# Optimization experiments

Hardware: AMD Instinct MI355X
Metric: run time of the kernel (lower is better)

Reference implementation:

```python
import jax, jax.numpy as jnp
import numpy as np

B, L, C = 4, 16384, 512   # batch, tokens (128x128 grid), dim
NH, WS = 8, 8             # num_heads, window grid (ws)
HD = C // NH              # head_dim = 64


def setup_inputs() -> dict:
    key = jax.random.key(0)
    k1, k2, k3, k4, k5 = jax.random.split(key, 5)
    return {
        "q":   jax.random.normal(k1, (B, L, C), dtype=jnp.float32),
        "kv":  jax.random.normal(k2, (B, L, C), dtype=jnp.float32),
        "Wq":  jax.random.normal(k3, (C, C), dtype=jnp.float32) * 0.02,
        "Wkv": jax.random.normal(k4, (C, 2 * C), dtype=jnp.float32) * 0.02,
        "Wfc": jax.random.normal(k5, (C, C), dtype=jnp.float32) * 0.02,
    }


def reference(q, kv, Wq, Wkv, Wfc):
    Bq, Lq, Cd = q.shape
    Lkv = kv.shape[1]
    nh, hd, ws = NH, Cd // NH, WS
    scale = hd ** (-0.5)
    hw_q = int(round(Lq ** 0.5))   # 128
    hw_k = int(round(Lkv ** 0.5))
    sq, sk = hw_q // ws, hw_k // ws  # window side lengths (16)

    qp = q @ Wq                                   # [B, Lq, C]
    kvp = (kv @ Wkv).reshape(Bq, Lkv, 2, Cd)
    k, v = kvp[:, :, 0], kvp[:, :, 1]             # [B, Lkv, C]

    def window(x, s):
        # [B, hw, hw, C] -> [B, ws*ws windows, heads, s*s tokens, hd]
        x = x.reshape(Bq, ws, s, ws, s, Cd).transpose(0, 1, 3, 2, 4, 5)
        x = x.reshape(Bq, ws * ws, s * s, nh, hd)
        return x.transpose(0, 1, 3, 2, 4)

    qw = window(qp, sq)   # [B, W, H, sq*sq, hd]
    kw = window(k, sk)    # [B, W, H, sk*sk, hd]
    vw = window(v, sk)

    attn = jnp.einsum('bwhqd,bwhkd->bwhqk', qw, kw) * scale
    attn = jax.nn.softmax(attn, axis=-1)
    o = jnp.einsum('bwhqk,bwhkd->bwhqd', attn, vw)  # [B, W, H, sq*sq, hd]

    # inverse window partition
    o = o.transpose(0, 1, 3, 2, 4).reshape(Bq, ws, ws, sq, sq, Cd)
    o = o.transpose(0, 1, 3, 2, 4, 5).reshape(Bq, Lq, Cd)
    return o @ Wfc
```

## Files before the change

kernel.cpp:

```cpp
#include <hip/hip_runtime.h>
#include <stdint.h>

#define BB 4
#define LL 16384
#define CC 512
#define MM (BB * LL)

typedef unsigned short u16;
typedef __bf16 bf16x8 __attribute__((ext_vector_type(8)));
typedef float f32x4 __attribute__((ext_vector_type(4)));
typedef u16 u16x8 __attribute__((ext_vector_type(8)));
typedef u16 u16x4 __attribute__((ext_vector_type(4)));

__device__ __forceinline__ u16 f2bf(float f) {
  return __builtin_bit_cast(u16, (__bf16)f);
}

__device__ __forceinline__ void gl_lds16(const void* g, void* l) {
  __builtin_amdgcn_global_load_lds((const __attribute__((address_space(1))) void*)g,
                                   (__attribute__((address_space(3))) void*)l,
                                   16, 0, 0);
}

__global__ __launch_bounds__(256) void prep_kernel(
    const float* __restrict__ q, const float* __restrict__ kv,
    const float* __restrict__ Wq, const float* __restrict__ Wkv,
    const float* __restrict__ Wfc, u16* __restrict__ qo, u16* __restrict__ kvo,
    u16* __restrict__ Wq_t, u16* __restrict__ Wkv_t, u16* __restrict__ Wfc_t) {
  __shared__ float tile[64][65];
  const int bid = blockIdx.x, tid = threadIdx.x;

  if (bid < 4096) {
    const int half = bid >> 11;
    const float* src = half ? kv : q;
    u16* dst = half ? kvo : qo;
    const int n16 = MM * CC / 16;
    const int stride = 2048 * 256;
    for (int i = (bid & 2047) * 256 + tid; i < n16; i += stride) {
      f32x4 a0 = reinterpret_cast<const f32x4*>(src)[4 * i + 0];
      f32x4 a1 = reinterpret_cast<const f32x4*>(src)[4 * i + 1];
      f32x4 a2 = reinterpret_cast<const f32x4*>(src)[4 * i + 2];
      f32x4 a3 = reinterpret_cast<const f32x4*>(src)[4 * i + 3];
      u16x8 o0, o1;
      o0[0] = f2bf(a0[0]); o0[1] = f2bf(a0[1]); o0[2] = f2bf(a0[2]); o0[3] = f2bf(a0[3]);
      o0[4] = f2bf(a1[0]); o0[5] = f2bf(a1[1]); o0[6] = f2bf(a1[2]); o0[7] = f2bf(a1[3]);
      o1[0] = f2bf(a2[0]); o1[1] = f2bf(a2[1]); o1[2] = f2bf(a2[2]); o1[3] = f2bf(a2[3]);
      o1[4] = f2bf(a3[0]); o1[5] = f2bf(a3[1]); o1[6] = f2bf(a3[2]); o1[7] = f2bf(a3[3]);
      reinterpret_cast<u16x8*>(dst)[2 * i + 0] = o0;
      reinterpret_cast<u16x8*>(dst)[2 * i + 1] = o1;
    }
    return;
  }

  const int wb = bid - 4096;
  const float* W; u16* Wt; int N, ti;
  if (wb < 64)       { W = Wq;  Wt = Wq_t;  N = 512;  ti = wb; }
  else if (wb < 192) { W = Wkv; Wt = Wkv_t; N = 1024; ti = wb - 64; }
  else               { W = Wfc; Wt = Wfc_t; N = 512;  ti = wb - 192; }
  const int ntn = N >> 6;
  const int kt = ti / ntn, nt = ti % ntn;
  const int k0 = kt << 6, n0 = nt << 6;
  {
    const int r = tid >> 4, c4 = tid & 15;
#pragma unroll
    for (int e = 0; e < 4; ++e) {
      int row = r + e * 16;
      f32x4 v = *reinterpret_cast<const f32x4*>(&W[(size_t)(k0 + row) * N + n0 + c4 * 4]);
      tile[row][c4 * 4 + 0] = v[0]; tile[row][c4 * 4 + 1] = v[1];
      tile[row][c4 * 4 + 2] = v[2]; tile[row][c4 * 4 + 3] = v[3];
    }
  }
  __syncthreads();
  {
    const int n = tid >> 2, qd = tid & 3;
#pragma unroll
    for (int e = 0; e < 2; ++e) {
      int c = qd * 2 + e;
      u16x8 o;
#pragma unroll
      for (int j = 0; j < 8; ++j) o[j] = f2bf(tile[c * 8 + j][n]);
      *reinterpret_cast<u16x8*>(&Wt[(size_t)(n0 + n) * 512 + k0 + c * 8]) = o;
    }
  }
}

template <bool OUT_F32>
__global__ __launch_bounds__(512, 2) void gemm256(const u16* __restrict__ A,
                                                  const u16* __restrict__ Bt,
                                                  void* __restrict__ Cp,
                                                  int M, int N, int K) {
  __shared__ __align__(16) u16 Al[3][16384];
  __shared__ __align__(16) u16 Bl[2][16384];
  const int nbn = N >> 8;
  const int nwg = gridDim.x;
  const int bid0 = blockIdx.x;
  const int cpx = nwg >> 3;
  const int bid = (bid0 & 7) * cpx + (bid0 >> 3);
  const int bm = bid / nbn, bn = bid % nbn;
  const size_t row0 = (size_t)bm << 8, col0 = (size_t)bn << 8;
  const int tid = threadIdx.x, lane = tid & 63;
  const int wv = tid >> 6, wm = wv >> 2, wn = wv & 3;
  const int ro = lane & 15, g4 = lane >> 4;
  const int NT = K >> 6;

  const int ci0 = tid, ci1 = tid + 512;
  const int r0 = ci0 >> 3, g0 = (ci0 & 7) ^ (r0 & 7);
  const int r1 = ci1 >> 3, g1 = (ci1 & 7) ^ (r1 & 7);

  auto stageA = [&](int half, int kt, u16* L) {
    gl_lds16(A + (row0 + half * 128 + r0) * (size_t)K + kt * 64 + g0 * 8, L + half * 8192 + ci0 * 8);
    gl_lds16(A + (row0 + half * 128 + r1) * (size_t)K + kt * 64 + g1 * 8, L + half * 8192 + ci1 * 8);
  };
  auto stageB = [&](int half, int kt, u16* L) {
    gl_lds16(Bt + (col0 + half * 128 + r0) * (size_t)K + kt * 64 + g0 * 8, L + half * 8192 + ci0 * 8);
    gl_lds16(Bt + (col0 + half * 128 + r1) * (size_t)K + kt * 64 + g1 * 8, L + half * 8192 + ci1 * 8);
  };

  const int aB = (wm * 128 + ro) * 64;
  const int bB = (wn * 64 + ro) * 64;
  const int sw0 = (g4 ^ (ro & 7)) * 8;
  const int sw1 = ((g4 + 4) ^ (ro & 7)) * 8;

  auto ldf = [&](const u16* p) { return *reinterpret_cast<const bf16x8*>(p); };

  f32x4 acc[8][4] = {};

  stageA(0, 0, Al[0]); stageA(1, 0, Al[0]);
  stageB(0, 0, Bl[0]); stageB(1, 0, Bl[0]);
  stageA(0, 1, Al[1]); stageA(1, 1, Al[1]);
  stageB(0, 1, Bl[1]); stageB(1, 1, Bl[1]);
  asm volatile("s_waitcnt vmcnt(8)" ::: "memory");
  __builtin_amdgcn_s_barrier();

  u16* Acur = Al[0]; u16* Anxt = Al[1]; u16* Asta = Al[2];
  u16* Bcur = Bl[0]; u16* Bnxt = Bl[1];

  for (int u = 0; u < NT; ++u) {
    const bool st = (u + 2) < NT;
    bf16x8 bfr[4][2], af[2][2];

#pragma unroll
    for (int n = 0; n < 4; ++n) {
      bfr[n][0] = ldf(Bcur + bB + n * 1024 + sw0);
      bfr[n][1] = ldf(Bcur + bB + n * 1024 + sw1);
    }
    af[0][0] = ldf(Acur + aB + sw0);        af[0][1] = ldf(Acur + aB + sw1);
    af[1][0] = ldf(Acur + aB + 1024 + sw0); af[1][1] = ldf(Acur + aB + 1024 + sw1);
    if (st) stageA(0, u + 2, Asta);
    __builtin_amdgcn_s_barrier();
    asm volatile("s_waitcnt lgkmcnt(0)" ::: "memory");
    __builtin_amdgcn_sched_barrier(0);
    __builtin_amdgcn_s_setprio(1);
#pragma unroll
    for (int m = 0; m < 2; ++m)
#pragma unroll
      for (int n = 0; n < 4; ++n) {
        acc[m][n] = __builtin_amdgcn_mfma_f32_16x16x32_bf16(af[m][0], bfr[n][0], acc[m][n], 0, 0, 0);
        acc[m][n] = __builtin_amdgcn_mfma_f32_16x16x32_bf16(af[m][1], bfr[n][1], acc[m][n], 0, 0, 0);
      }
    __builtin_amdgcn_s_setprio(0);
    __builtin_amdgcn_s_barrier();

#pragma unroll
    for (int ph = 1; ph < 4; ++ph) {
      af[0][0] = ldf(Acur + aB + (2 * ph) * 1024 + sw0);
      af[0][1] = ldf(Acur + aB + (2 * ph) * 1024 + sw1);
      af[1][0] = ldf(Acur + aB + (2 * ph + 1) * 1024 + sw0);
      af[1][1] = ldf(Acur + aB + (2 * ph + 1) * 1024 + sw1);
      if (ph == 1) { if (st) { stageA(1, u + 2, Asta); stageB(0, u + 2, Bcur); } }
      else if (ph == 2) { if (st) stageB(1, u + 2, Bcur); }
      __builtin_amdgcn_s_barrier();
      asm volatile("s_waitcnt lgkmcnt(0)" ::: "memory");
      __builtin_amdgcn_sched_barrier(0);
      __builtin_amdgcn_s_setprio(1);
#pragma unroll
      for (int m = 0; m < 2; ++m)
#pragma unroll
        for (int n = 0; n < 4; ++n) {
          acc[2 * ph + m][n] =
              __builtin_amdgcn_mfma_f32_16x16x32_bf16(af[m][0], bfr[n][0], acc[2 * ph + m][n], 0, 0, 0);
          acc[2 * ph + m][n] =
              __builtin_amdgcn_mfma_f32_16x16x32_bf16(af[m][1], bfr[n][1], acc[2 * ph + m][n], 0, 0, 0);
        }
      __builtin_amdgcn_s_setprio(0);
      if (ph == 3) {
        if (st) asm volatile("s_waitcnt vmcnt(8)" ::: "memory");
        else    asm volatile("s_waitcnt vmcnt(0)" ::: "memory");
      }
      __builtin_amdgcn_s_barrier();
    }

    u16* ta = Acur; Acur = Anxt; Anxt = Asta; Asta = ta;
    u16* tb = Bcur; Bcur = Bnxt; Bnxt = tb;
  }

#pragma unroll
  for (int m = 0; m < 8; ++m)
#pragma unroll
    for (int n = 0; n < 4; ++n)
#pragma unroll
      for (int j = 0; j < 4; ++j) {
        size_t r = row0 + wm * 128 + m * 16 + g4 * 4 + j;
        size_t c = col0 + wn * 64 + n * 16 + ro;
        if (OUT_F32)
          reinterpret_cast<float*>(Cp)[r * N + c] = acc[m][n][j];
        else
          reinterpret_cast<u16*>(Cp)[r * N + c] = f2bf(acc[m][n][j]);
      }
}

__global__ __launch_bounds__(512, 4) void attn_kernel(const u16* __restrict__ qp,
                                                      const u16* __restrict__ kvp,
                                                      u16* __restrict__ o) {
  __shared__ __align__(16) u16 Kl[256 * 64];
  __shared__ __align__(16) u16 Vt[64 * 256];
  __shared__ __align__(16) u16 Pl[8 * 1024];
  const int bid = blockIdx.x;
  const int h = bid & 7, w = (bid >> 3) & 63, b = bid >> 9;
  const int w1 = w >> 3, w2 = w & 7;
  const int tid = threadIdx.x, lane = tid & 63, wv = tid >> 6;

  auto lrow = [&](int t) { return (w1 * 16 + (t >> 4)) * 128 + w2 * 16 + (t & 15); };

#pragma unroll
  for (int p = 0; p < 4; ++p) {
    int ci = tid + p * 512;
    int r = ci >> 3, g = (ci & 7) ^ (r & 7);
    gl_lds16(kvp + ((size_t)(b * LL + lrow(r))) * 1024 + h * 64 + g * 8, Kl + ci * 8);
  }
  {
    const int tk = tid >> 1, half = tid & 1;
    const size_t base = ((size_t)(b * LL + lrow(tk))) * 1024 + 512 + h * 64 + half * 32;
#pragma unroll
    for (int c = 0; c < 4; ++c) {
      u16x8 vx = *reinterpret_cast<const u16x8*>(kvp + base + c * 8);
#pragma unroll
      for (int e = 0; e < 8; ++e) {
        int d = half * 32 + c * 8 + e;
        Vt[d * 256 + (((tk >> 3) ^ (d & 7)) * 8) + (tk & 7)] = vx[e];
      }
    }
  }
  __syncthreads();

  const int ro = lane & 15;
  const int g4 = lane >> 4;
  const float scale = 0.125f;
  const int swA = (g4 ^ (ro & 7)) * 8;
  const int swB = ((g4 + 4) ^ (ro & 7)) * 8;
  u16* PW = Pl + wv * 1024;

  auto ldf = [&](const u16* p) { return *reinterpret_cast<const bf16x8*>(p); };

#pragma unroll
  for (int rt = 0; rt < 2; ++rt) {
    const int tq = 32 * wv + 16 * rt + ro;
    const size_t qbase = ((size_t)(b * LL + lrow(tq))) * 512 + h * 64 + g4 * 8;
    const bf16x8 qf0 = *reinterpret_cast<const bf16x8*>(qp + qbase);
    const bf16x8 qf1 = *reinterpret_cast<const bf16x8*>(qp + qbase + 32);

    f32x4 sa[16] = {};
    __builtin_amdgcn_s_setprio(1);
#pragma unroll
    for (int ct = 0; ct < 16; ++ct) {
      bf16x8 kf0 = ldf(Kl + (16 * ct + ro) * 64 + swA);
      bf16x8 kf1 = ldf(Kl + (16 * ct + ro) * 64 + swB);
      sa[ct] = __builtin_amdgcn_mfma_f32_16x16x32_bf16(qf0, kf0, sa[ct], 0, 0, 0);
      sa[ct] = __builtin_amdgcn_mfma_f32_16x16x32_bf16(qf1, kf1, sa[ct], 0, 0, 0);
    }
    __builtin_amdgcn_s_setprio(0);

#pragma unroll
    for (int j = 0; j < 4; ++j) {
      float m = -1e30f;
#pragma unroll
      for (int ct = 0; ct < 16; ++ct) m = fmaxf(m, sa[ct][j]);
      m = fmaxf(m, __shfl_xor(m, 1));
      m = fmaxf(m, __shfl_xor(m, 2));
      m = fmaxf(m, __shfl_xor(m, 4));
      m = fmaxf(m, __shfl_xor(m, 8));
      m *= scale;
      float s = 0.f;
#pragma unroll
      for (int ct = 0; ct < 16; ++ct) {
        float p = __expf(sa[ct][j] * scale - m);
        sa[ct][j] = p;
        s += p;
      }
      s += __shfl_xor(s, 1);
      s += __shfl_xor(s, 2);
      s += __shfl_xor(s, 4);
      s += __shfl_xor(s, 8);
      float inv = 1.f / s;
#pragma unroll
      for (int ct = 0; ct < 16; ++ct) sa[ct][j] *= inv;
    }

    f32x4 oacc[4] = {};
#pragma unroll
    for (int kh = 0; kh < 4; ++kh) {
#pragma unroll
      for (int c = 0; c < 4; ++c)
#pragma unroll
        for (int j = 0; j < 4; ++j) {
          int rq = g4 * 4 + j;
          PW[rq * 64 + (((2 * c + (ro >> 3)) ^ (rq & 7)) * 8) + (ro & 7)] =
              f2bf(sa[kh * 4 + c][j]);
        }
      __builtin_amdgcn_s_setprio(1);
#pragma unroll
      for (int ks = 0; ks < 2; ++ks) {
        bf16x8 pf = ldf(PW + ro * 64 + (((ks * 4 + g4) ^ (ro & 7)) * 8));
        const int kkg = kh * 2 + ks;
#pragma unroll
        for (int cd = 0; cd < 4; ++cd) {
          bf16x8 vf = ldf(Vt + (16 * cd + ro) * 256 + (((kkg * 4 + g4) ^ (ro & 7)) * 8));
          oacc[cd] = __builtin_amdgcn_mfma_f32_16x16x32_bf16(pf, vf, oacc[cd], 0, 0, 0);
        }
      }
      __builtin_amdgcn_s_setprio(0);
    }

#pragma unroll
    for (int cd = 0; cd < 4; ++cd)
#pragma unroll
      for (int j = 0; j < 4; ++j) {
        int t = 32 * wv + 16 * rt + g4 * 4 + j;
        int d = 16 * cd + ro;
        o[((size_t)(b * LL + lrow(t))) * 512 + h * 64 + d] = f2bf(oacc[cd][j]);
      }
  }
}

extern "C" void kernel_launch(void* const* d_in, const int* in_sizes, int n_in,
                              void* d_out, int out_size, void* d_ws, size_t ws_size,
                              hipStream_t stream) {
  const float* q = (const float*)d_in[0];
  const float* kv = (const float*)d_in[1];
  const float* Wq = (const float*)d_in[2];
  const float* Wkv = (const float*)d_in[3];
  const float* Wfc = (const float*)d_in[4];
  float* out = (float*)d_out;
  char* ws = (char*)d_ws;

  u16* q_bf  = (u16*)(ws + 0);
  u16* kv_bf = (u16*)(ws + 67108864);
  u16* qp    = (u16*)(ws + 134217728);
  u16* kvp   = (u16*)(ws + 201326592);
  u16* Wq_t  = (u16*)(ws + 335544320);
  u16* Wkv_t = (u16*)(ws + 336068608);
  u16* Wfc_t = (u16*)(ws + 337117184);
  u16* o_buf = q_bf;

  prep_kernel<<<4352, 256, 0, stream>>>(q, kv, Wq, Wkv, Wfc, q_bf, kv_bf, Wq_t, Wkv_t, Wfc_t);

  gemm256<false><<<(MM / 256) * (CC / 256), 512, 0, stream>>>(q_bf, Wq_t, qp, MM, CC, CC);
  gemm256<false><<<(MM / 256) * (2 * CC / 256), 512, 0, stream>>>(kv_bf, Wkv_t, kvp, MM, 2 * CC, CC);

  attn_kernel<<<BB * 64 * 8, 512, 0, stream>>>(qp, kvp, o_buf);

  gemm256<true><<<(MM / 256) * (CC / 256), 512, 0, stream>>>(o_buf, Wfc_t, out, MM, CC, CC);
}
```

Before: 356.3 us.

## Make GEMM persistent with cross-tile prefetch pipeline and nontemporal prep loads

The GEMM kernel becomes persistent: 256 workgroups each process several consecutive output tiles. The LDS prefetch pipeline now continues across tile boundaries, so loads for the next tile's first k-steps overlap the current tile's tail and epilogue. This removes per-tile launch and prologue/drain bubbles. It also hard-codes K=512, which limits generality. Separately, the fp32→bf16 conversion in the prep kernel uses nontemporal loads to avoid polluting the cache with streaming input.

```diff
diff --git a/kernel.cpp b/kernel.cpp
--- a/kernel.cpp
+++ b/kernel.cpp
@@ -37,10 +37,11 @@
     const int n16 = MM * CC / 16;
     const int stride = 2048 * 256;
     for (int i = (bid & 2047) * 256 + tid; i < n16; i += stride) {
-      f32x4 a0 = reinterpret_cast<const f32x4*>(src)[4 * i + 0];
-      f32x4 a1 = reinterpret_cast<const f32x4*>(src)[4 * i + 1];
-      f32x4 a2 = reinterpret_cast<const f32x4*>(src)[4 * i + 2];
-      f32x4 a3 = reinterpret_cast<const f32x4*>(src)[4 * i + 3];
+      const f32x4* sp = reinterpret_cast<const f32x4*>(src) + 4 * i;
+      f32x4 a0 = __builtin_nontemporal_load(sp + 0);
+      f32x4 a1 = __builtin_nontemporal_load(sp + 1);
+      f32x4 a2 = __builtin_nontemporal_load(sp + 2);
+      f32x4 a3 = __builtin_nontemporal_load(sp + 3);
       u16x8 o0, o1;
       o0[0] = f2bf(a0[0]); o0[1] = f2bf(a0[1]); o0[2] = f2bf(a0[2]); o0[3] = f2bf(a0[3]);
       o0[4] = f2bf(a1[0]); o0[5] = f2bf(a1[1]); o0[6] = f2bf(a1[2]); o0[7] = f2bf(a1[3]);
@@ -88,32 +89,30 @@
 __global__ __launch_bounds__(512, 2) void gemm256(const u16* __restrict__ A,
                                                   const u16* __restrict__ Bt,
                                                   void* __restrict__ Cp,
-                                                  int M, int N, int K) {
+                                                  int N, int TPB, int nbnl) {
+  constexpr int K = 512;
+  constexpr int NT = 8;
   __shared__ __align__(16) u16 Al[3][16384];
   __shared__ __align__(16) u16 Bl[2][16384];
-  const int nbn = N >> 8;
-  const int nwg = gridDim.x;
   const int bid0 = blockIdx.x;
-  const int cpx = nwg >> 3;
-  const int bid = (bid0 & 7) * cpx + (bid0 >> 3);
-  const int bm = bid / nbn, bn = bid % nbn;
-  const size_t row0 = (size_t)bm << 8, col0 = (size_t)bn << 8;
+  const int bid = (bid0 & 7) * 32 + (bid0 >> 3);
+  const int T0 = bid * TPB;
+  const int taumax = TPB * NT;
   const int tid = threadIdx.x, lane = tid & 63;
   const int wv = tid >> 6, wm = wv >> 2, wn = wv & 3;
   const int ro = lane & 15, g4 = lane >> 4;
-  const int NT = K >> 6;
 
   const int ci0 = tid, ci1 = tid + 512;
   const int r0 = ci0 >> 3, g0 = (ci0 & 7) ^ (r0 & 7);
   const int r1 = ci1 >> 3, g1 = (ci1 & 7) ^ (r1 & 7);
 
-  auto stageA = [&](int half, int kt, u16* L) {
-    gl_lds16(A + (row0 + half * 128 + r0) * (size_t)K + kt * 64 + g0 * 8, L + half * 8192 + ci0 * 8);
-    gl_lds16(A + (row0 + half * 128 + r1) * (size_t)K + kt * 64 + g1 * 8, L + half * 8192 + ci1 * 8);
+  auto stageA = [&](int half, size_t row0s, int us, u16* L) {
+    gl_lds16(A + (row0s + half * 128 + r0) * (size_t)K + us * 64 + g0 * 8, L + half * 8192 + ci0 * 8);
+    gl_lds16(A + (row0s + half * 128 + r1) * (size_t)K + us * 64 + g1 * 8, L + half * 8192 + ci1 * 8);
   };
-  auto stageB = [&](int half, int kt, u16* L) {
-    gl_lds16(Bt + (col0 + half * 128 + r0) * (size_t)K + kt * 64 + g0 * 8, L + half * 8192 + ci0 * 8);
-    gl_lds16(Bt + (col0 + half * 128 + r1) * (size_t)K + kt * 64 + g1 * 8, L + half * 8192 + ci1 * 8);
+  auto stageB = [&](int half, size_t col0s, int us, u16* L) {
+    gl_lds16(Bt + (col0s + half * 128 + r0) * (size_t)K + us * 64 + g0 * 8, L + half * 8192 + ci0 * 8);
+    gl_lds16(Bt + (col0s + half * 128 + r1) * (size_t)K + us * 64 + g1 * 8, L + half * 8192 + ci1 * 8);
   };
 
   const int aB = (wm * 128 + ro) * 64;
@@ -122,53 +121,43 @@
   const int sw1 = ((g4 + 4) ^ (ro & 7)) * 8;
 
   auto ldf = [&](const u16* p) { return *reinterpret_cast<const bf16x8*>(p); };
+  auto trow = [&](int T) { return (size_t)(T >> nbnl) << 8; };
+  auto tcol = [&](int T) { return (size_t)(T & ((1 << nbnl) - 1)) << 8; };
 
   f32x4 acc[8][4] = {};
 
-  stageA(0, 0, Al[0]); stageA(1, 0, Al[0]);
-  stageB(0, 0, Bl[0]); stageB(1, 0, Bl[0]);
-  stageA(0, 1, Al[1]); stageA(1, 1, Al[1]);
-  stageB(0, 1, Bl[1]); stageB(1, 1, Bl[1]);
+  {
+    size_t sr = trow(T0), sc = tcol(T0);
+    stageA(0, sr, 0, Al[0]); stageA(1, sr, 0, Al[0]);
+    stageB(0, sc, 0, Bl[0]); stageB(1, sc, 0, Bl[0]);
+    stageA(0, sr, 1, Al[1]); stageA(1, sr, 1, Al[1]);
+    stageB(0, sc, 1, Bl[1]); stageB(1, sc, 1, Bl[1]);
+  }
   asm volatile("s_waitcnt vmcnt(8)" ::: "memory");
   __builtin_amdgcn_s_barrier();
 
-  u16* Acur = Al[0]; u16* Anxt = Al[1]; u16* Asta = Al[2];
-  u16* Bcur = Bl[0]; u16* Bnxt = Bl[1];
-
-  for (int u = 0; u < NT; ++u) {
-    const bool st = (u + 2) < NT;
-    bf16x8 bfr[4][2], af[2][2];
-
-#pragma unroll
-    for (int n = 0; n < 4; ++n) {
-      bfr[n][0] = ldf(Bcur + bB + n * 1024 + sw0);
-      bfr[n][1] = ldf(Bcur + bB + n * 1024 + sw1);
-    }
-    af[0][0] = ldf(Acur + aB + sw0);        af[0][1] = ldf(Acur + aB + sw1);
-    af[1][0] = ldf(Acur + aB + 1024 + sw0); af[1][1] = ldf(Acur + aB + 1024 + sw1);
-    if (st) stageA(0, u + 2, Asta);
-    __builtin_amdgcn_s_barrier();
-    asm volatile("s_waitcnt lgkmcnt(0)" ::: "memory");
-    __builtin_amdgcn_sched_barrier(0);
-    __builtin_amdgcn_s_setprio(1);
-#pragma unroll
-    for (int m = 0; m < 2; ++m)
+  u16 *Acur = Al[0], *Anxt = Al[1], *Asta = Al[2];
+  u16 *Bcur = Bl[0], *Bnxt = Bl[1];
+
+  int tau = 0;
+  for (int T = T0; T < T0 + TPB; ++T) {
+    const size_t erow0 = trow(T), ecol0 = tcol(T);
+    for (int u = 0; u < NT; ++u, ++tau) {
+      const int tau2 = tau + 2;
+      const bool st = tau2 < taumax;
+      const int us = tau2 & 7;
+      const int T2 = T0 + (tau2 >> 3);
+      const size_t srow0 = trow(T2), scol0 = tcol(T2);
+      bf16x8 bfr[4][2], af[2][2];
+
 #pragma unroll
       for (int n = 0; n < 4; ++n) {
-        acc[m][n] = __builtin_amdgcn_mfma_f32_16x16x32_bf16(af[m][0], bfr[n][0], acc[m][n], 0, 0, 0);
-        acc[m][n] = __builtin_amdgcn_mfma_f32_16x16x32_bf16(af[m][1], bfr[n][1], acc[m][n], 0, 0, 0);
-      }
-    __builtin_amdgcn_s_setprio(0);
-    __builtin_amdgcn_s_barrier();
-
-#pragma unroll
-    for (int ph = 1; ph < 4; ++ph) {
-      af[0][0] = ldf(Acur + aB + (2 * ph) * 1024 + sw0);
-      af[0][1] = ldf(Acur + aB + (2 * ph) * 1024 + sw1);
-      af[1][0] = ldf(Acur + aB + (2 * ph + 1) * 1024 + sw0);
-      af[1][1] = ldf(Acur + aB + (2 * ph + 1) * 1024 + sw1);
-      if (ph == 1) { if (st) { stageA(1, u + 2, Asta); stageB(0, u + 2, Bcur); } }
-      else if (ph == 2) { if (st) stageB(1, u + 2, Bcur); }
+        bfr[n][0] = ldf(Bcur + bB + n * 1024 + sw0);
+        bfr[n][1] = ldf(Bcur + bB + n * 1024 + sw1);
+      }
+      af[0][0] = ldf(Acur + aB + sw0);        af[0][1] = ldf(Acur + aB + sw1);
+      af[1][0] = ldf(Acur + aB + 1024 + sw0); af[1][1] = ldf(Acur + aB + 1024 + sw1);
+      if (st) stageA(0, srow0, us, Asta);
       __builtin_amdgcn_s_barrier();
       asm volatile("s_waitcnt lgkmcnt(0)" ::: "memory");
       __builtin_amdgcn_sched_barrier(0);
@@ -177,36 +166,61 @@
       for (int m = 0; m < 2; ++m)
 #pragma unroll
         for (int n = 0; n < 4; ++n) {
-          acc[2 * ph + m][n] =
-              __builtin_amdgcn_mfma_f32_16x16x32_bf16(af[m][0], bfr[n][0], acc[2 * ph + m][n], 0, 0, 0);
-          acc[2 * ph + m][n] =
-              __builtin_amdgcn_mfma_f32_16x16x32_bf16(af[m][1], bfr[n][1], acc[2 * ph + m][n], 0, 0, 0);
+          acc[m][n] = __builtin_amdgcn_mfma_f32_16x16x32_bf16(af[m][0], bfr[n][0], acc[m][n], 0, 0, 0);
+          acc[m][n] = __builtin_amdgcn_mfma_f32_16x16x32_bf16(af[m][1], bfr[n][1], acc[m][n], 0, 0, 0);
         }
       __builtin_amdgcn_s_setprio(0);
-      if (ph == 3) {
-        if (st) asm volatile("s_waitcnt vmcnt(8)" ::: "memory");
-        else    asm volatile("s_waitcnt vmcnt(0)" ::: "memory");
-      }
       __builtin_amdgcn_s_barrier();
-    }
-
-    u16* ta = Acur; Acur = Anxt; Anxt = Asta; Asta = ta;
-    u16* tb = Bcur; Bcur = Bnxt; Bnxt = tb;
-  }
-
-#pragma unroll
-  for (int m = 0; m < 8; ++m)
-#pragma unroll
-    for (int n = 0; n < 4; ++n)
-#pragma unroll
-      for (int j = 0; j < 4; ++j) {
-        size_t r = row0 + wm * 128 + m * 16 + g4 * 4 + j;
-        size_t c = col0 + wn * 64 + n * 16 + ro;
-        if (OUT_F32)
-          reinterpret_cast<float*>(Cp)[r * N + c] = acc[m][n][j];
-        else
-          reinterpret_cast<u16*>(Cp)[r * N + c] = f2bf(acc[m][n][j]);
-      }
+
+#pragma unroll
+      for (int ph = 1; ph < 4; ++ph) {
+        af[0][0] = ldf(Acur + aB + (2 * ph) * 1024 + sw0);
+        af[0][1] = ldf(Acur + aB + (2 * ph) * 1024 + sw1);
+        af[1][0] = ldf(Acur + aB + (2 * ph + 1) * 1024 + sw0);
+        af[1][1] = ldf(Acur + aB + (2 * ph + 1) * 1024 + sw1);
+        if (ph == 1) { if (st) { stageA(1, srow0, us, Asta); stageB(0, scol0, us, Bcur); } }
+        else if (ph == 2) { if (st) stageB(1, scol0, us, Bcur); }
+        __builtin_amdgcn_s_barrier();
+        asm volatile("s_waitcnt lgkmcnt(0)" ::: "memory");
+        __builtin_amdgcn_sched_barrier(0);
+        __builtin_amdgcn_s_setprio(1);
+#pragma unroll
+        for (int m = 0; m < 2; ++m)
+#pragma unroll
+          for (int n = 0; n < 4; ++n) {
+            acc[2 * ph + m][n] =
+                __builtin_amdgcn_mfma_f32_16x16x32_bf16(af[m][0], bfr[n][0], acc[2 * ph + m][n], 0, 0, 0);
+            acc[2 * ph + m][n] =
+                __builtin_amdgcn_mfma_f32_16x16x32_bf16(af[m][1], bfr[n][1], acc[2 * ph + m][n], 0, 0, 0);
+          }
+        __builtin_amdgcn_s_setprio(0);
+        if (ph == 3) {
+          if (st) asm volatile("s_waitcnt vmcnt(8)" ::: "memory");
+          else    asm volatile("s_waitcnt vmcnt(0)" ::: "memory");
+        }
+        __builtin_amdgcn_s_barrier();
+      }
+
+      u16* ta = Acur; Acur = Anxt; Anxt = Asta; Asta = ta;
+      u16* tb = Bcur; Bcur = Bnxt; Bnxt = tb;
+    }
+
+#pragma unroll
+    for (int m = 0; m < 8; ++m)
+#pragma unroll
+      for (int n = 0; n < 4; ++n) {
+#pragma unroll
+        for (int j = 0; j < 4; ++j) {
+          size_t r = erow0 + wm * 128 + m * 16 + g4 * 4 + j;
+          size_t c = ecol0 + wn * 64 + n * 16 + ro;
+          if (OUT_F32)
+            reinterpret_cast<float*>(Cp)[r * N + c] = acc[m][n][j];
+          else
+            reinterpret_cast<u16*>(Cp)[r * N + c] = f2bf(acc[m][n][j]);
+        }
+        acc[m][n] = (f32x4){0.f, 0.f, 0.f, 0.f};
+      }
+  }
 }
 
 __global__ __launch_bounds__(512, 4) void attn_kernel(const u16* __restrict__ qp,
@@ -354,10 +368,10 @@
 
   prep_kernel<<<4352, 256, 0, stream>>>(q, kv, Wq, Wkv, Wfc, q_bf, kv_bf, Wq_t, Wkv_t, Wfc_t);
 
-  gemm256<false><<<(MM / 256) * (CC / 256), 512, 0, stream>>>(q_bf, Wq_t, qp, MM, CC, CC);
-  gemm256<false><<<(MM / 256) * (2 * CC / 256), 512, 0, stream>>>(kv_bf, Wkv_t, kvp, MM, 2 * CC, CC);
+  gemm256<false><<<256, 512, 0, stream>>>(q_bf, Wq_t, qp, CC, 2, 1);
+  gemm256<false><<<256, 512, 0, stream>>>(kv_bf, Wkv_t, kvp, 2 * CC, 4, 2);
 
   attn_kernel<<<BB * 64 * 8, 512, 0, stream>>>(qp, kvp, o_buf);
 
-  gemm256<true><<<(MM / 256) * (CC / 256), 512, 0, stream>>>(o_buf, Wfc_t, out, MM, CC, CC);
-}
+  gemm256<true><<<256, 512, 0, stream>>>(o_buf, Wfc_t, out, CC, 2, 1);
+}
```

Measured after the change: 385.1 us. +8.1%, slower.
